# Kernel optimization log

Measured on AMD Instinct MI355X. Metric: run time of the kernel, lower is better.

Reference implementation:

```python
import jax, jax.numpy as jnp
import numpy as np

B, T, D, U = 64, 2048, 256, 256

def setup_inputs() -> dict:
    key = jax.random.key(0)
    ks = jax.random.split(key, 8)
    return {
        "query": jax.random.normal(ks[0], (B, D), dtype=jnp.float32),
        "values": jax.random.normal(ks[1], (B, T, D), dtype=jnp.float32),
        "W1_w": jax.random.normal(ks[2], (D, U), dtype=jnp.float32) * 0.05,
        "W1_b": jnp.zeros((U,), dtype=jnp.float32),
        "W2_w": jax.random.normal(ks[3], (D, U), dtype=jnp.float32) * 0.05,
        "W2_b": jnp.zeros((U,), dtype=jnp.float32),
        "V_w": jax.random.normal(ks[4], (U, 1), dtype=jnp.float32) * 0.05,
        "V_b": jnp.zeros((1,), dtype=jnp.float32),
    }

def reference(query, values, W1_w, W1_b, W2_w, W2_b, V_w, V_b):
    # query: [B, D] -> [B, 1, U]
    q_proj = (query @ W1_w + W1_b)[:, None, :]
    # values: [B, T, D] -> [B, T, U]
    v_proj = jnp.einsum('btd,du->btu', values, W2_w) + W2_b
    # score: [B, T, 1]
    score = jnp.tanh(q_proj + v_proj) @ V_w + V_b
    attention_weights = jax.nn.softmax(score, axis=1)  # over time axis
    context_vector = jnp.sum(attention_weights * values, axis=1)  # [B, D]
    return (context_vector, attention_weights)
```

## Files before the change

kernel.cpp:

```cpp
#include <hip/hip_runtime.h>
#include <stdint.h>

#define B_ 64
#define T_ 2048
#define D_ 256
#define U_ 256
#define BT 256
#define NT (BT / 16)
#define TC (T_ / BT)
#define SHIFT_ 8.0f

typedef _Float16 half8   __attribute__((ext_vector_type(8)));
typedef float    floatx4 __attribute__((ext_vector_type(4)));

typedef const __attribute__((address_space(1))) void cg_void;
typedef __attribute__((address_space(3))) void       ls_void;

__global__ void qproj_kernel(const float* __restrict__ query,
                             const float* __restrict__ W1_w,
                             const float* __restrict__ W1_b,
                             const float* __restrict__ W2_b,
                             float* __restrict__ qb) {
    __shared__ float qrow[D_];
    const int b = blockIdx.x;
    const int u = threadIdx.x;
    qrow[u] = query[b * D_ + u];
    __syncthreads();
    float a0 = 0.f, a1 = 0.f, a2 = 0.f, a3 = 0.f;
#pragma unroll 4
    for (int d = 0; d < D_; d += 4) {
        a0 += qrow[d    ] * W1_w[(d    ) * U_ + u];
        a1 += qrow[d + 1] * W1_w[(d + 1) * U_ + u];
        a2 += qrow[d + 2] * W1_w[(d + 2) * U_ + u];
        a3 += qrow[d + 3] * W1_w[(d + 3) * U_ + u];
    }
    qb[b * U_ + u] = (a0 + a1) + (a2 + a3) + W1_b[u] + W2_b[u];
}

__global__ void w2t_kernel(const float* __restrict__ W2_w, _Float16* __restrict__ w2t) {
    __shared__ float tile[32][33];
    const int tu = blockIdx.x & 7;
    const int td = blockIdx.x >> 3;
    const int c  = threadIdx.x & 31;
    const int r0 = threadIdx.x >> 5;
#pragma unroll
    for (int i = 0; i < 4; ++i) {
        int r = r0 + i * 8;
        tile[r][c] = W2_w[(td * 32 + r) * U_ + tu * 32 + c];
    }
    __syncthreads();
#pragma unroll
    for (int i = 0; i < 4; ++i) {
        int r = r0 + i * 8;
        w2t[(tu * 32 + r) * D_ + td * 32 + c] = (_Float16)tile[c][r];
    }
}

__launch_bounds__(256, 2)
__global__ void score_ctx_kernel(const float* __restrict__ values,
                                 const _Float16* __restrict__ w2t,
                                 const float* __restrict__ qb,
                                 const float* __restrict__ V_w,
                                 float* __restrict__ scores,
                                 float* __restrict__ pctx,
                                 float* __restrict__ pl) {
    __shared__ __align__(16) float buf[3][16 * D_];
    __shared__ __align__(16) float s_part2[16][4];
    __shared__ float sbuf[BT];

    const int b     = blockIdx.y;
    const int chunk = blockIdx.x;
    const int tid   = threadIdx.x;
    const int wave  = tid >> 6;
    const int lane  = tid & 63;
    const int n16   = lane & 15;
    const int quad  = lane >> 4;
    const int u0    = wave * 64;

    half8 bfrag[4][8];
#pragma unroll
    for (int ut = 0; ut < 4; ++ut) {
        const int u = u0 + ut * 16 + n16;
#pragma unroll
        for (int k = 0; k < 8; ++k)
            bfrag[ut][k] = *(const half8*)(w2t + u * D_ + k * 32 + quad * 8);
    }
    float qbv[4], vwv[4];
#pragma unroll
    for (int ut = 0; ut < 4; ++ut) {
        const int u = u0 + ut * 16 + n16;
        qbv[ut] = qb[b * U_ + u];
        vwv[ut] = V_w[u];
    }

    const float* vbase = values + (size_t)b * T_ * D_ + (size_t)chunk * BT * D_;

    const int e0 = (quad * 2) ^ (n16 & 7);
    const int e1 = e0 ^ 1;

    const int g = tid >> 2, lo = tid & 3;
    int co[8];
#pragma unroll
    for (int s = 0; s < 8; ++s) co[s] = (((g ^ s) & 63) << 2) + lo;

    float c = 0.f;
    float l = 0.f;

    auto stage = [&](int tile, int bi) {
        const float* src = vbase + tile * 16 * D_;
#pragma unroll
        for (int i = 0; i < 4; ++i) {
            const int r = i * 4 + wave;
            const float* gp = src + r * D_ + ((lane ^ (r & 7)) << 2);
            float* lp = &buf[bi][r * D_];
            __builtin_amdgcn_global_load_lds((cg_void*)gp, (ls_void*)lp, 16, 0, 0);
        }
    };

    stage(0, 0);
    stage(1, 1);

    int cur = 0;
#pragma unroll 1
    for (int tile = 0; tile < NT; ++tile) {
        if (tile < NT - 1) asm volatile("s_waitcnt vmcnt(4) lgkmcnt(0)" ::: "memory");
        else               asm volatile("s_waitcnt vmcnt(0) lgkmcnt(0)" ::: "memory");
        __builtin_amdgcn_s_barrier();
        asm volatile("" ::: "memory");

        const int nx = (cur == 0) ? 2 : cur - 1;
        if (tile + 2 < NT) stage(tile + 2, nx);

        const float* a0p = &buf[cur][n16 * D_] + (e0 << 2);
        const float* a1p = &buf[cur][n16 * D_] + (e1 << 2);
        floatx4 acc[4] = {};
#pragma unroll
        for (int k = 0; k < 8; ++k) {
            floatx4 q0 = *(const floatx4*)(a0p + (k << 5));
            floatx4 q1 = *(const floatx4*)(a1p + (k << 5));
            half8 a;
            a[0] = (_Float16)q0.x; a[1] = (_Float16)q0.y;
            a[2] = (_Float16)q0.z; a[3] = (_Float16)q0.w;
            a[4] = (_Float16)q1.x; a[5] = (_Float16)q1.y;
            a[6] = (_Float16)q1.z; a[7] = (_Float16)q1.w;
#pragma unroll
            for (int ut = 0; ut < 4; ++ut)
                acc[ut] = __builtin_amdgcn_mfma_f32_16x16x32_f16(a, bfrag[ut][k], acc[ut], 0, 0, 0);
        }

        float part[4];
#pragma unroll
        for (int r = 0; r < 4; ++r) {
            float s = 0.f;
#pragma unroll
            for (int ut = 0; ut < 4; ++ut) {
                float x  = acc[ut][r] + qbv[ut];
                float e  = __expf(2.f * x);
                float th = 1.f - __fdividef(2.f, e + 1.f);
                s += th * vwv[ut];
            }
            part[r] = s;
        }
#pragma unroll
        for (int m = 1; m < 16; m <<= 1)
#pragma unroll
            for (int r = 0; r < 4; ++r)
                part[r] += __shfl_xor(part[r], m, 16);
        if (n16 == 0) {
#pragma unroll
            for (int r = 0; r < 4; ++r)
                s_part2[quad * 4 + r][wave] = part[r];
        }

        asm volatile("s_waitcnt lgkmcnt(0)" ::: "memory");
        __builtin_amdgcn_s_barrier();
        asm volatile("" ::: "memory");

        const float* bufp = &buf[cur][0];
        const float* sp2  = &s_part2[0][0];
#pragma unroll
        for (int t = 0; t < 16; ++t) {
            floatx4 sp = *(const floatx4*)(sp2 + t * 4);
            float s = (sp.x + sp.y) + (sp.z + sp.w);
            float w = __expf(s - SHIFT_);
            l += w;
            c += w * bufp[t * D_ + co[t & 7]];
        }
        if (tid < 16) {
            floatx4 sp = *(const floatx4*)(sp2 + tid * 4);
            sbuf[tile * 16 + tid] = (sp.x + sp.y) + (sp.z + sp.w);
        }

        cur = (cur == 2) ? 0 : cur + 1;
    }

    __syncthreads();
    pctx[(b * TC + chunk) * D_ + tid] = c;
    scores[b * T_ + chunk * BT + tid] = sbuf[tid];
    if (tid == 0) pl[b * TC + chunk] = l;
}

__global__ void finalize_kernel(const float* __restrict__ pctx,
                                const float* __restrict__ pl,
                                const float* __restrict__ scores,
                                float* __restrict__ ctx,
                                float* __restrict__ attn) {
    const int b = blockIdx.x, tid = threadIdx.x;
    float L = 0.f;
#pragma unroll
    for (int i = 0; i < TC; ++i) L += pl[b * TC + i];
    float s = 0.f;
#pragma unroll
    for (int i = 0; i < TC; ++i) s += pctx[(b * TC + i) * D_ + tid];
    const float invL = __fdividef(1.f, L);
    ctx[b * D_ + tid] = s * invL;
#pragma unroll
    for (int j = 0; j < T_ / 256; ++j) {
        const int t = j * 256 + tid;
        attn[b * T_ + t] = __expf(scores[b * T_ + t] - SHIFT_) * invL;
    }
}

extern "C" void kernel_launch(void* const* d_in, const int* in_sizes, int n_in,
                              void* d_out, int out_size, void* d_ws, size_t ws_size,
                              hipStream_t stream) {
    const float* query  = (const float*)d_in[0];
    const float* values = (const float*)d_in[1];
    const float* W1_w   = (const float*)d_in[2];
    const float* W1_b   = (const float*)d_in[3];
    const float* W2_w   = (const float*)d_in[4];
    const float* W2_b   = (const float*)d_in[5];
    const float* V_w    = (const float*)d_in[6];

    float* out  = (float*)d_out;
    float* ctx  = out;
    float* attn = out + B_ * D_;

    char* ws = (char*)d_ws;
    float*    qb     = (float*)ws;
    _Float16* w2t    = (_Float16*)(ws + (64 << 10));
    float*    scores = (float*)(ws + (192 << 10));
    float*    pctx   = (float*)(ws + (704 << 10));
    float*    pl     = (float*)(ws + (1216 << 10));

    qproj_kernel    <<<dim3(B_),      dim3(256), 0, stream>>>(query, W1_w, W1_b, W2_b, qb);
    w2t_kernel      <<<dim3(64),      dim3(256), 0, stream>>>(W2_w, w2t);
    score_ctx_kernel<<<dim3(TC, B_),  dim3(256), 0, stream>>>(values, w2t, qb, V_w, scores, pctx, pl);
    finalize_kernel <<<dim3(B_),      dim3(256), 0, stream>>>(pctx, pl, scores, ctx, attn);
}
```

Before: 239.2 us.

## Stage values as fp16 in LDS via registers, halve chunk size, merge prep kernels

Replaces the direct global-to-LDS fp32 staging with register-prefetched loads that are converted to fp16 before being written into a swizzled double buffer. This cuts LDS footprint and allows more resident blocks per CU, with launch bounds raised from 2 to 4. BT drops from 256 to 128, doubling the grid and the number of partial context rows. The qproj and W2-transpose kernels are merged into one launch. The context accumulation now reads fp16-rounded values, which loses precision, and the register staging adds VGPR pressure.

```diff
diff --git a/kernel.cpp b/kernel.cpp
--- a/kernel.cpp
+++ b/kernel.cpp
@@ -5,58 +5,59 @@
 #define T_ 2048
 #define D_ 256
 #define U_ 256
-#define BT 256
+#define BT 128
 #define NT (BT / 16)
 #define TC (T_ / BT)
 #define SHIFT_ 8.0f
 
 typedef _Float16 half8   __attribute__((ext_vector_type(8)));
+typedef _Float16 halfx4  __attribute__((ext_vector_type(4)));
 typedef float    floatx4 __attribute__((ext_vector_type(4)));
 
-typedef const __attribute__((address_space(1))) void cg_void;
-typedef __attribute__((address_space(3))) void       ls_void;
-
-__global__ void qproj_kernel(const float* __restrict__ query,
-                             const float* __restrict__ W1_w,
-                             const float* __restrict__ W1_b,
-                             const float* __restrict__ W2_b,
-                             float* __restrict__ qb) {
+__global__ void prep_kernel(const float* __restrict__ query,
+                            const float* __restrict__ W1_w,
+                            const float* __restrict__ W1_b,
+                            const float* __restrict__ W2_b,
+                            const float* __restrict__ W2_w,
+                            float* __restrict__ qb,
+                            _Float16* __restrict__ w2t) {
     __shared__ float qrow[D_];
-    const int b = blockIdx.x;
-    const int u = threadIdx.x;
-    qrow[u] = query[b * D_ + u];
-    __syncthreads();
-    float a0 = 0.f, a1 = 0.f, a2 = 0.f, a3 = 0.f;
+    __shared__ float tile[32][33];
+    if (blockIdx.x < 64) {
+        const int b = blockIdx.x;
+        const int u = threadIdx.x;
+        qrow[u] = query[b * D_ + u];
+        __syncthreads();
+        float a0 = 0.f, a1 = 0.f, a2 = 0.f, a3 = 0.f;
 #pragma unroll 4
-    for (int d = 0; d < D_; d += 4) {
-        a0 += qrow[d    ] * W1_w[(d    ) * U_ + u];
-        a1 += qrow[d + 1] * W1_w[(d + 1) * U_ + u];
-        a2 += qrow[d + 2] * W1_w[(d + 2) * U_ + u];
-        a3 += qrow[d + 3] * W1_w[(d + 3) * U_ + u];
-    }
-    qb[b * U_ + u] = (a0 + a1) + (a2 + a3) + W1_b[u] + W2_b[u];
-}
-
-__global__ void w2t_kernel(const float* __restrict__ W2_w, _Float16* __restrict__ w2t) {
-    __shared__ float tile[32][33];
-    const int tu = blockIdx.x & 7;
-    const int td = blockIdx.x >> 3;
-    const int c  = threadIdx.x & 31;
-    const int r0 = threadIdx.x >> 5;
-#pragma unroll
-    for (int i = 0; i < 4; ++i) {
-        int r = r0 + i * 8;
-        tile[r][c] = W2_w[(td * 32 + r) * U_ + tu * 32 + c];
-    }
-    __syncthreads();
-#pragma unroll
-    for (int i = 0; i < 4; ++i) {
-        int r = r0 + i * 8;
-        w2t[(tu * 32 + r) * D_ + td * 32 + c] = (_Float16)tile[c][r];
-    }
-}
-
-__launch_bounds__(256, 2)
+        for (int d = 0; d < D_; d += 4) {
+            a0 += qrow[d    ] * W1_w[(d    ) * U_ + u];
+            a1 += qrow[d + 1] * W1_w[(d + 1) * U_ + u];
+            a2 += qrow[d + 2] * W1_w[(d + 2) * U_ + u];
+            a3 += qrow[d + 3] * W1_w[(d + 3) * U_ + u];
+        }
+        qb[b * U_ + u] = (a0 + a1) + (a2 + a3) + W1_b[u] + W2_b[u];
+    } else {
+        const int bid = blockIdx.x - 64;
+        const int tu = bid & 7;
+        const int td = bid >> 3;
+        const int c  = threadIdx.x & 31;
+        const int r0 = threadIdx.x >> 5;
+#pragma unroll
+        for (int i = 0; i < 4; ++i) {
+            int r = r0 + i * 8;
+            tile[r][c] = W2_w[(td * 32 + r) * U_ + tu * 32 + c];
+        }
+        __syncthreads();
+#pragma unroll
+        for (int i = 0; i < 4; ++i) {
+            int r = r0 + i * 8;
+            w2t[(tu * 32 + r) * D_ + td * 32 + c] = (_Float16)tile[c][r];
+        }
+    }
+}
+
+__launch_bounds__(256, 4)
 __global__ void score_ctx_kernel(const float* __restrict__ values,
                                  const _Float16* __restrict__ w2t,
                                  const float* __restrict__ qb,
@@ -64,7 +65,7 @@
                                  float* __restrict__ scores,
                                  float* __restrict__ pctx,
                                  float* __restrict__ pl) {
-    __shared__ __align__(16) float buf[3][16 * D_];
+    __shared__ __align__(16) _Float16 buf[2][16 * D_];
     __shared__ __align__(16) float s_part2[16][4];
     __shared__ float sbuf[BT];
 
@@ -95,71 +96,80 @@
 
     const float* vbase = values + (size_t)b * T_ * D_ + (size_t)chunk * BT * D_;
 
-    const int e0 = (quad * 2) ^ (n16 & 7);
-    const int e1 = e0 ^ 1;
-
-    const int g = tid >> 2, lo = tid & 3;
-    int co[8];
-#pragma unroll
-    for (int s = 0; s < 8; ++s) co[s] = (((g ^ s) & 63) << 2) + lo;
+    const int s3   = n16 & 3;
+    const int sb2  = (n16 >> 2) & 1;
+    const int abase = n16 * 512 + (quad ^ s3) * 16;
+    const int A0 = abase + (sb2 ? 64 : 0);
+    const int A1 = abase + (sb2 ? 0 : 64);
+
+    const int ob0 = ((tid >> 3) << 4) + (tid & 7) * 2;
+
+    const int wp  = ((lane >> 1) << 4) + (lane & 1) * 8 + wave * 512;
+    const int wwA = (wp & ~(15 << 4)) | ((((lane >> 1) ^ wave) & 31) << 4);
+    const int wwB = (wp & ~(15 << 4)) | ((((lane >> 1) ^ (wave + 4)) & 31) << 4);
 
     float c = 0.f;
     float l = 0.f;
 
-    auto stage = [&](int tile, int bi) {
-        const float* src = vbase + tile * 16 * D_;
-#pragma unroll
-        for (int i = 0; i < 4; ++i) {
-            const int r = i * 4 + wave;
-            const float* gp = src + r * D_ + ((lane ^ (r & 7)) << 2);
-            float* lp = &buf[bi][r * D_];
-            __builtin_amdgcn_global_load_lds((cg_void*)gp, (ls_void*)lp, 16, 0, 0);
-        }
+    floatx4 st0, st1, st2, st3;
+
+    auto loadst = [&](int t) {
+        const float* p = vbase + (size_t)(t * 16 + wave) * D_ + lane * 4;
+        st0 = *(const floatx4*)(p);
+        st1 = *(const floatx4*)(p + 4 * D_);
+        st2 = *(const floatx4*)(p + 8 * D_);
+        st3 = *(const floatx4*)(p + 12 * D_);
     };
-
-    stage(0, 0);
-    stage(1, 1);
-
-    int cur = 0;
+    auto writest = [&](int bi) {
+        char* dstb = (char*)&buf[bi][0];
+        halfx4 h;
+        h[0] = (_Float16)st0.x; h[1] = (_Float16)st0.y; h[2] = (_Float16)st0.z; h[3] = (_Float16)st0.w;
+        *(halfx4*)(dstb + wwA + 0 * 2048) = h;
+        h[0] = (_Float16)st1.x; h[1] = (_Float16)st1.y; h[2] = (_Float16)st1.z; h[3] = (_Float16)st1.w;
+        *(halfx4*)(dstb + wwB + 1 * 2048) = h;
+        h[0] = (_Float16)st2.x; h[1] = (_Float16)st2.y; h[2] = (_Float16)st2.z; h[3] = (_Float16)st2.w;
+        *(halfx4*)(dstb + wwA + 2 * 2048) = h;
+        h[0] = (_Float16)st3.x; h[1] = (_Float16)st3.y; h[2] = (_Float16)st3.z; h[3] = (_Float16)st3.w;
+        *(halfx4*)(dstb + wwB + 3 * 2048) = h;
+    };
+
+    loadst(0);
+    writest(0);
+    loadst(1);
+
 #pragma unroll 1
     for (int tile = 0; tile < NT; ++tile) {
-        if (tile < NT - 1) asm volatile("s_waitcnt vmcnt(4) lgkmcnt(0)" ::: "memory");
-        else               asm volatile("s_waitcnt vmcnt(0) lgkmcnt(0)" ::: "memory");
+        const int cur = tile & 1;
+        asm volatile("s_waitcnt lgkmcnt(0)" ::: "memory");
         __builtin_amdgcn_s_barrier();
         asm volatile("" ::: "memory");
 
-        const int nx = (cur == 0) ? 2 : cur - 1;
-        if (tile + 2 < NT) stage(tile + 2, nx);
-
-        const float* a0p = &buf[cur][n16 * D_] + (e0 << 2);
-        const float* a1p = &buf[cur][n16 * D_] + (e1 << 2);
+        const char* slotp = (const char*)&buf[cur][0];
         floatx4 acc[4] = {};
 #pragma unroll
-        for (int k = 0; k < 8; ++k) {
-            floatx4 q0 = *(const floatx4*)(a0p + (k << 5));
-            floatx4 q1 = *(const floatx4*)(a1p + (k << 5));
-            half8 a;
-            a[0] = (_Float16)q0.x; a[1] = (_Float16)q0.y;
-            a[2] = (_Float16)q0.z; a[3] = (_Float16)q0.w;
-            a[4] = (_Float16)q1.x; a[5] = (_Float16)q1.y;
-            a[6] = (_Float16)q1.z; a[7] = (_Float16)q1.w;
+        for (int m = 0; m < 4; ++m) {
+            half8 a0 = *(const half8*)(slotp + A0 + m * 128);
+            half8 a1 = *(const half8*)(slotp + A1 + m * 128);
 #pragma unroll
             for (int ut = 0; ut < 4; ++ut)
-                acc[ut] = __builtin_amdgcn_mfma_f32_16x16x32_f16(a, bfrag[ut][k], acc[ut], 0, 0, 0);
+                acc[ut] = __builtin_amdgcn_mfma_f32_16x16x32_f16(a0, bfrag[ut][2 * m], acc[ut], 0, 0, 0);
+#pragma unroll
+            for (int ut = 0; ut < 4; ++ut)
+                acc[ut] = __builtin_amdgcn_mfma_f32_16x16x32_f16(a1, bfrag[ut][2 * m + 1], acc[ut], 0, 0, 0);
         }
 
         float part[4];
 #pragma unroll
         for (int r = 0; r < 4; ++r) {
-            float s = 0.f;
+            float sa = 0.f;
 #pragma unroll
             for (int ut = 0; ut < 4; ++ut) {
                 float x  = acc[ut][r] + qbv[ut];
                 float e  = __expf(2.f * x);
                 float th = 1.f - __fdividef(2.f, e + 1.f);
-                s += th * vwv[ut];
+                sa += th * vwv[ut];
             }
-            part[r] = s;
+            part[r] = sa;
         }
 #pragma unroll
         for (int m = 1; m < 16; m <<= 1)
@@ -176,27 +186,28 @@
         __builtin_amdgcn_s_barrier();
         asm volatile("" ::: "memory");
 
-        const float* bufp = &buf[cur][0];
-        const float* sp2  = &s_part2[0][0];
+        if (tile + 1 < NT) writest(cur ^ 1);
+        if (tile + 2 < NT) loadst(tile + 2);
+
+        const float* sp2 = &s_part2[0][0];
 #pragma unroll
         for (int t = 0; t < 16; ++t) {
             floatx4 sp = *(const floatx4*)(sp2 + t * 4);
-            float s = (sp.x + sp.y) + (sp.z + sp.w);
-            float w = __expf(s - SHIFT_);
+            float sv = (sp.x + sp.y) + (sp.z + sp.w);
+            float w  = __expf(sv - SHIFT_);
             l += w;
-            c += w * bufp[t * D_ + co[t & 7]];
+            float v = (float)*(const _Float16*)(slotp + t * 512 + (ob0 ^ ((t & 7) << 4)));
+            c += w * v;
         }
         if (tid < 16) {
             floatx4 sp = *(const floatx4*)(sp2 + tid * 4);
             sbuf[tile * 16 + tid] = (sp.x + sp.y) + (sp.z + sp.w);
         }
-
-        cur = (cur == 2) ? 0 : cur + 1;
     }
 
     __syncthreads();
     pctx[(b * TC + chunk) * D_ + tid] = c;
-    scores[b * T_ + chunk * BT + tid] = sbuf[tid];
+    if (tid < BT) scores[b * T_ + chunk * BT + tid] = sbuf[tid];
     if (tid == 0) pl[b * TC + chunk] = l;
 }
 
@@ -241,10 +252,9 @@
     _Float16* w2t    = (_Float16*)(ws + (64 << 10));
     float*    scores = (float*)(ws + (192 << 10));
     float*    pctx   = (float*)(ws + (704 << 10));
-    float*    pl     = (float*)(ws + (1216 << 10));
-
-    qproj_kernel    <<<dim3(B_),      dim3(256), 0, stream>>>(query, W1_w, W1_b, W2_b, qb);
-    w2t_kernel      <<<dim3(64),      dim3(256), 0, stream>>>(W2_w, w2t);
+    float*    pl     = (float*)(ws + (1728 << 10));
+
+    prep_kernel     <<<dim3(128),     dim3(256), 0, stream>>>(query, W1_w, W1_b, W2_b, W2_w, qb, w2t);
     score_ctx_kernel<<<dim3(TC, B_),  dim3(256), 0, stream>>>(values, w2t, qb, V_w, scores, pctx, pl);
     finalize_kernel <<<dim3(B_),      dim3(256), 0, stream>>>(pctx, pl, scores, ctx, attn);
 }
```

Measured after the change: 386.3 us. 1.62x slower.

## Halve time chunk size, double-buffer staging, and merge prep kernels

Applied to the files above, without the earlier changes.

Cuts the per-block time chunk from 256 to 128 rows, which doubles the grid to 1024 blocks for more parallelism. It drops LDS from triple to double buffering, so more blocks can be resident, and waits for all loads before each tile. The query projection and W2 transpose kernels merge into one launch to save launch overhead. The cost is less load/compute overlap per block, twice as many partial context rows for finalize to reduce, and a relocated pl workspace offset.

```diff
diff --git a/kernel.cpp b/kernel.cpp
--- a/kernel.cpp
+++ b/kernel.cpp
@@ -5,7 +5,7 @@
 #define T_ 2048
 #define D_ 256
 #define U_ 256
-#define BT 256
+#define BT 128
 #define NT (BT / 16)
 #define TC (T_ / BT)
 #define SHIFT_ 8.0f
@@ -16,43 +16,46 @@
 typedef const __attribute__((address_space(1))) void cg_void;
 typedef __attribute__((address_space(3))) void       ls_void;
 
-__global__ void qproj_kernel(const float* __restrict__ query,
-                             const float* __restrict__ W1_w,
-                             const float* __restrict__ W1_b,
-                             const float* __restrict__ W2_b,
-                             float* __restrict__ qb) {
+__global__ void prep_kernel(const float* __restrict__ query,
+                            const float* __restrict__ W1_w,
+                            const float* __restrict__ W1_b,
+                            const float* __restrict__ W2_b,
+                            const float* __restrict__ W2_w,
+                            float* __restrict__ qb,
+                            _Float16* __restrict__ w2t) {
     __shared__ float qrow[D_];
-    const int b = blockIdx.x;
-    const int u = threadIdx.x;
-    qrow[u] = query[b * D_ + u];
-    __syncthreads();
-    float a0 = 0.f, a1 = 0.f, a2 = 0.f, a3 = 0.f;
+    __shared__ float tile[32][33];
+    if (blockIdx.x < 64) {
+        const int b = blockIdx.x;
+        const int u = threadIdx.x;
+        qrow[u] = query[b * D_ + u];
+        __syncthreads();
+        float a0 = 0.f, a1 = 0.f, a2 = 0.f, a3 = 0.f;
 #pragma unroll 4
-    for (int d = 0; d < D_; d += 4) {
-        a0 += qrow[d    ] * W1_w[(d    ) * U_ + u];
-        a1 += qrow[d + 1] * W1_w[(d + 1) * U_ + u];
-        a2 += qrow[d + 2] * W1_w[(d + 2) * U_ + u];
-        a3 += qrow[d + 3] * W1_w[(d + 3) * U_ + u];
-    }
-    qb[b * U_ + u] = (a0 + a1) + (a2 + a3) + W1_b[u] + W2_b[u];
-}
-
-__global__ void w2t_kernel(const float* __restrict__ W2_w, _Float16* __restrict__ w2t) {
-    __shared__ float tile[32][33];
-    const int tu = blockIdx.x & 7;
-    const int td = blockIdx.x >> 3;
-    const int c  = threadIdx.x & 31;
-    const int r0 = threadIdx.x >> 5;
-#pragma unroll
-    for (int i = 0; i < 4; ++i) {
-        int r = r0 + i * 8;
-        tile[r][c] = W2_w[(td * 32 + r) * U_ + tu * 32 + c];
-    }
-    __syncthreads();
-#pragma unroll
-    for (int i = 0; i < 4; ++i) {
-        int r = r0 + i * 8;
-        w2t[(tu * 32 + r) * D_ + td * 32 + c] = (_Float16)tile[c][r];
+        for (int d = 0; d < D_; d += 4) {
+            a0 += qrow[d    ] * W1_w[(d    ) * U_ + u];
+            a1 += qrow[d + 1] * W1_w[(d + 1) * U_ + u];
+            a2 += qrow[d + 2] * W1_w[(d + 2) * U_ + u];
+            a3 += qrow[d + 3] * W1_w[(d + 3) * U_ + u];
+        }
+        qb[b * U_ + u] = (a0 + a1) + (a2 + a3) + W1_b[u] + W2_b[u];
+    } else {
+        const int bid = blockIdx.x - 64;
+        const int tu = bid & 7;
+        const int td = bid >> 3;
+        const int c  = threadIdx.x & 31;
+        const int r0 = threadIdx.x >> 5;
+#pragma unroll
+        for (int i = 0; i < 4; ++i) {
+            int r = r0 + i * 8;
+            tile[r][c] = W2_w[(td * 32 + r) * U_ + tu * 32 + c];
+        }
+        __syncthreads();
+#pragma unroll
+        for (int i = 0; i < 4; ++i) {
+            int r = r0 + i * 8;
+            w2t[(tu * 32 + r) * D_ + td * 32 + c] = (_Float16)tile[c][r];
+        }
     }
 }
 
@@ -64,7 +67,7 @@
                                  float* __restrict__ scores,
                                  float* __restrict__ pctx,
                                  float* __restrict__ pl) {
-    __shared__ __align__(16) float buf[3][16 * D_];
+    __shared__ __align__(16) float buf[2][16 * D_];
     __shared__ __align__(16) float s_part2[16][4];
     __shared__ float sbuf[BT];
 
@@ -118,18 +121,15 @@
     };
 
     stage(0, 0);
-    stage(1, 1);
-
-    int cur = 0;
+
 #pragma unroll 1
     for (int tile = 0; tile < NT; ++tile) {
-        if (tile < NT - 1) asm volatile("s_waitcnt vmcnt(4) lgkmcnt(0)" ::: "memory");
-        else               asm volatile("s_waitcnt vmcnt(0) lgkmcnt(0)" ::: "memory");
+        const int cur = tile & 1;
+        asm volatile("s_waitcnt vmcnt(0) lgkmcnt(0)" ::: "memory");
         __builtin_amdgcn_s_barrier();
         asm volatile("" ::: "memory");
 
-        const int nx = (cur == 0) ? 2 : cur - 1;
-        if (tile + 2 < NT) stage(tile + 2, nx);
+        if (tile + 1 < NT) stage(tile + 1, cur ^ 1);
 
         const float* a0p = &buf[cur][n16 * D_] + (e0 << 2);
         const float* a1p = &buf[cur][n16 * D_] + (e1 << 2);
@@ -151,15 +151,15 @@
         float part[4];
 #pragma unroll
         for (int r = 0; r < 4; ++r) {
-            float s = 0.f;
+            float sa = 0.f;
 #pragma unroll
             for (int ut = 0; ut < 4; ++ut) {
                 float x  = acc[ut][r] + qbv[ut];
                 float e  = __expf(2.f * x);
                 float th = 1.f - __fdividef(2.f, e + 1.f);
-                s += th * vwv[ut];
+                sa += th * vwv[ut];
             }
-            part[r] = s;
+            part[r] = sa;
         }
 #pragma unroll
         for (int m = 1; m < 16; m <<= 1)
@@ -181,8 +181,8 @@
 #pragma unroll
         for (int t = 0; t < 16; ++t) {
             floatx4 sp = *(const floatx4*)(sp2 + t * 4);
-            float s = (sp.x + sp.y) + (sp.z + sp.w);
-            float w = __expf(s - SHIFT_);
+            float sv = (sp.x + sp.y) + (sp.z + sp.w);
+            float w  = __expf(sv - SHIFT_);
             l += w;
             c += w * bufp[t * D_ + co[t & 7]];
         }
@@ -190,13 +190,11 @@
             floatx4 sp = *(const floatx4*)(sp2 + tid * 4);
             sbuf[tile * 16 + tid] = (sp.x + sp.y) + (sp.z + sp.w);
         }
-
-        cur = (cur == 2) ? 0 : cur + 1;
     }
 
     __syncthreads();
     pctx[(b * TC + chunk) * D_ + tid] = c;
-    scores[b * T_ + chunk * BT + tid] = sbuf[tid];
+    if (tid < BT) scores[b * T_ + chunk * BT + tid] = sbuf[tid];
     if (tid == 0) pl[b * TC + chunk] = l;
 }
 
@@ -241,10 +239,9 @@
     _Float16* w2t    = (_Float16*)(ws + (64 << 10));
     float*    scores = (float*)(ws + (192 << 10));
     float*    pctx   = (float*)(ws + (704 << 10));
-    float*    pl     = (float*)(ws + (1216 << 10));
-
-    qproj_kernel    <<<dim3(B_),      dim3(256), 0, stream>>>(query, W1_w, W1_b, W2_b, qb);
-    w2t_kernel      <<<dim3(64),      dim3(256), 0, stream>>>(W2_w, w2t);
+    float*    pl     = (float*)(ws + (1728 << 10));
+
+    prep_kernel     <<<dim3(128),     dim3(256), 0, stream>>>(query, W1_w, W1_b, W2_b, W2_w, qb, w2t);
     score_ctx_kernel<<<dim3(TC, B_),  dim3(256), 0, stream>>>(values, w2t, qb, V_w, scores, pctx, pl);
     finalize_kernel <<<dim3(B_),      dim3(256), 0, stream>>>(pctx, pl, scores, ctx, attn);
 }
```

New measurement: 240.0 us. Within noise of the previous version (+0.3%).
